# Optimization experiments

Hardware: AMD Instinct MI355X
Metric: run time of the kernel (lower is better)

The kernel has to match this reference:

```python
import jax, jax.numpy as jnp
import numpy as np

MARGIN = 0.5

def setup_inputs() -> dict:
    key = jax.random.key(0)
    k1, k2, k3, k4 = jax.random.split(key, 4)
    B, C, T, K = 16, 512, 2048, 4096
    student_out = jax.random.normal(k1, (B, C, T), dtype=jnp.float32)
    teacher_out = jax.random.normal(k2, (B, C, T), dtype=jnp.float32)
    codebook = jax.random.normal(k3, (K, C), dtype=jnp.float32)
    teacher_codes = jax.random.randint(k4, (B, T), 0, K, dtype=jnp.int64)
    return {"student_out": student_out, "teacher_out": teacher_out,
            "codebook": codebook, "teacher_codes": teacher_codes}

def _hard_negatives(student_out, codebook, teacher_codes):
    B, C, T = student_out.shape
    z = jnp.transpose(student_out, (0, 2, 1)).reshape(-1, C)  # (B*T, C)
    # squared Euclidean via expansion; sqrt-free suffices for argmin but keep faithful masking
    sq = (jnp.sum(z * z, axis=1, keepdims=True)
          + jnp.sum(codebook * codebook, axis=1)[None, :]
          - 2.0 * z @ codebook.T)                              # (B*T, K)
    dists = jnp.sqrt(jnp.maximum(sq, 0.0))
    tflat = teacher_codes.reshape(-1)
    rows = jnp.arange(tflat.shape[0])
    dists = dists.at[rows, tflat].set(jnp.inf)                 # mask correct code
    hard_idx = jnp.argmin(dists, axis=1)                       # (B*T,)
    return codebook[hard_idx].reshape(B, T, C)

def reference(student_out, teacher_out, codebook, teacher_codes):
    B, C, T = student_out.shape
    negative = _hard_negatives(student_out, codebook, teacher_codes)  # (B, T, C)
    anchor = jnp.transpose(teacher_out, (0, 2, 1))   # (B, T, C)
    positive = jnp.transpose(student_out, (0, 2, 1)) # (B, T, C)
    d_pos = jnp.linalg.norm(anchor - positive, axis=-1)  # (B, T)
    d_neg = jnp.linalg.norm(anchor - negative, axis=-1)  # (B, T)
    losses = jax.nn.relu(d_pos - d_neg + MARGIN)
    loss = losses.mean()
    d_pos_mean = d_pos.mean()
    d_neg_mean = d_neg.mean()
    margin_satisfied = (d_neg > d_pos + MARGIN).astype(jnp.float32).mean()
    return (loss, d_pos_mean, d_neg_mean, margin_satisfied)
```

## Files before the change

### kernel.cpp

```cpp
#include <hip/hip_runtime.h>
#include <math.h>

#define B_ 16
#define C_ 512
#define T_ 2048
#define K_ 4096
#define M_ (B_*T_)
#define MARGIN_ 0.5f

typedef float f32x4    __attribute__((ext_vector_type(4)));
typedef int   int32x4v __attribute__((ext_vector_type(4)));
typedef int   int32x8v __attribute__((ext_vector_type(8)));

static __device__ __forceinline__ unsigned int umin_(unsigned int a, unsigned int b) {
    return a < b ? a : b;
}
static __device__ __forceinline__ unsigned int umax_(unsigned int a, unsigned int b) {
    return a > b ? a : b;
}
static __device__ __forceinline__ void gload_lds16(const void* g, void* l) {
    __builtin_amdgcn_global_load_lds(
        (const __attribute__((address_space(1))) unsigned int*)g,
        (__attribute__((address_space(3))) unsigned int*)l,
        16, 0, 0);
}

static __device__ __forceinline__ unsigned char f32_to_e4m3(float x) {
    unsigned int u = __float_as_uint(x);
    unsigned int sgn = (u >> 24) & 0x80u;
    unsigned int ax = u & 0x7FFFFFFFu;
    if (ax >= 0x43E00000u) return (unsigned char)(sgn | 0x7Eu);
    if (ax < 0x3C800000u) {
        int q = (int)rintf(__uint_as_float(ax) * 512.0f);
        if (q >= 8) return (unsigned char)(sgn | 0x08u);
        return (unsigned char)(sgn | (unsigned)q);
    }
    unsigned int b = ax + 0x7FFFFu + ((ax >> 20) & 1u);
    unsigned int e = b >> 23;
    unsigned int m = (b >> 20) & 7u;
    int e4 = (int)e - 127 + 7;
    if (e4 >= 16) return (unsigned char)(sgn | 0x7Eu);
    return (unsigned char)(sgn | ((unsigned)e4 << 3) | m);
}

static __device__ __forceinline__ int kperm8(int o) {
    int g  = o >> 7;
    int r  = o & 127;
    int s  = (r >> 5) & 3;
    int h  = (r >> 4) & 1;
    int b8 = (r >> 3) & 1;
    return g * 128 + h * 64 + s * 16 + b8 * 8;
}

__global__ __launch_bounds__(256) void packA_kernel(
    const float* __restrict__ student, unsigned char* __restrict__ Apack)
{
    __shared__ float ts[64][65];
    const int tid = threadIdx.x;
    const int t0 = blockIdx.x * 64;
    const int c0 = blockIdx.y * 64;
    const int b  = blockIdx.z;

#pragma unroll
    for (int r = 0; r < 4; ++r) {
        int f  = tid + r * 256;
        int i  = f >> 4;
        int j4 = (f & 15) << 2;
        float4 v = *reinterpret_cast<const float4*>(
            student + ((size_t)(b * C_ + c0 + i)) * T_ + (t0 + j4));
        *reinterpret_cast<float4*>(&ts[i][j4]) = v;
    }
    __syncthreads();

#pragma unroll
    for (int r = 0; r < 2; ++r) {
        int f  = tid + r * 256;
        int j  = f >> 3;
        int pi = f & 7;
        unsigned long long w = 0ull;
#pragma unroll
        for (int u = 0; u < 8; ++u) {
            unsigned long long byte8 = (unsigned long long)f32_to_e4m3(ts[pi * 8 + u][j]);
            w |= byte8 << (8 * u);
        }
        *reinterpret_cast<unsigned long long*>(
            Apack + (size_t)(b * T_ + t0 + j) * 512 + kperm8(c0 + pi * 8)) = w;
    }
}

__global__ __launch_bounds__(256) void packB_norm_kernel(
    const float* __restrict__ cb, unsigned char* __restrict__ Bpack,
    float* __restrict__ cbnb256)
{
    int code = blockIdx.x * 4 + (threadIdx.x >> 6);
    int lane = threadIdx.x & 63;
    const float* row = cb + (size_t)code * C_;
    unsigned char* orow = Bpack + (size_t)code * 512;

    int c = lane * 8;
    float4 v0 = *reinterpret_cast<const float4*>(row + c);
    float4 v1 = *reinterpret_cast<const float4*>(row + c + 4);
    float s = v0.x*v0.x + v0.y*v0.y + v0.z*v0.z + v0.w*v0.w
            + v1.x*v1.x + v1.y*v1.y + v1.z*v1.z + v1.w*v1.w;
    unsigned long long w =
          (unsigned long long)f32_to_e4m3(v0.x)
        | ((unsigned long long)f32_to_e4m3(v0.y) << 8)
        | ((unsigned long long)f32_to_e4m3(v0.z) << 16)
        | ((unsigned long long)f32_to_e4m3(v0.w) << 24)
        | ((unsigned long long)f32_to_e4m3(v1.x) << 32)
        | ((unsigned long long)f32_to_e4m3(v1.y) << 40)
        | ((unsigned long long)f32_to_e4m3(v1.z) << 48)
        | ((unsigned long long)f32_to_e4m3(v1.w) << 56);
    *reinterpret_cast<unsigned long long*>(orow + kperm8(c)) = w;

#pragma unroll
    for (int off = 32; off; off >>= 1) s += __shfl_down(s, off);
    if (lane == 0) cbnb256[code] = (s + 1024.0f) * 256.0f;
}

__global__ __launch_bounds__(256, 2) void screen_kernel(
    const unsigned char* __restrict__ Apack,
    const unsigned char* __restrict__ Bpack,
    const float* __restrict__ cbnb256,
    uint2* __restrict__ out2)
{
    __shared__ __align__(16) unsigned char lds_tiles[4 * 2 * 128 * 64];
    __shared__ float cbnb_lds[1024];

    const int tid = threadIdx.x;
    const int l   = tid & 63;
    const int wv  = tid >> 6;
    const int wm  = wv >> 1, wn = wv & 1;
    const int lr  = l & 15;
    const int lk  = l >> 4;

    const int bid = blockIdx.x;
    const int wg  = (bid & 7) * 128 + (bid >> 3);
    const int q   = wg & 3;
    const int m0  = (wg >> 2) * 128;

    {
        float4 v = reinterpret_cast<const float4*>(cbnb256 + q * 1024)[tid];
        reinterpret_cast<float4*>(cbnb_lds)[tid] = v;
    }

    unsigned int u1[16], u2v[16];
#pragma unroll
    for (int e = 0; e < 16; ++e) { u1[e] = 0xFFFFFFFFu; u2v[e] = 0xFFFFFFFFu; }

    f32x4 acc[4][4];
#pragma unroll
    for (int i = 0; i < 4; ++i)
#pragma unroll
        for (int j = 0; j < 4; ++j) acc[i][j] = (f32x4)0.f;

    const int lane_goff = (l >> 2) * 512 + (((l & 3) ^ ((l >> 3) & 3)) * 16);
    const int r0 = wv * 32, r1 = wv * 32 + 16;

    const char* pA0 = (const char*)Apack + (size_t)m0 * 512 + lane_goff + (size_t)r0 * 512;
    const char* pA1 = (const char*)Apack + (size_t)m0 * 512 + lane_goff + (size_t)r1 * 512;
    const char* pB0 = (const char*)Bpack + (size_t)q * 524288 + lane_goff + (size_t)r0 * 512;
    const char* pB1 = (const char*)Bpack + (size_t)q * 524288 + lane_goff + (size_t)r1 * 512;

    auto stage_ptr = [&](unsigned bufbase) {
        unsigned char* Ad = &lds_tiles[bufbase];
        unsigned char* Bd = &lds_tiles[bufbase + 8192];
        gload_lds16(pA0, Ad + r0 * 64);
        gload_lds16(pA1, Ad + r1 * 64);
        gload_lds16(pB0, Bd + r0 * 64);
        gload_lds16(pB1, Bd + r1 * 64);
    };
    auto advance = [&](int s_next) {
        bool wrap = (s_next & 7) == 0;
        int dA = wrap ? -448 : 64;
        int dB = wrap ? 65088 : 64;
        pA0 += dA; pA1 += dA; pB0 += dB; pB1 += dB;
    };

    const int slotoff = (lk ^ ((lr >> 1) & 3)) * 16;

    auto compute_window = [&](unsigned bufL, unsigned bufH) {
        int32x8v a[4], bb[4];
#pragma unroll
        for (int i = 0; i < 4; ++i) {
            int ar = wm * 64 + i * 16 + lr;
            int32x4v lo = *reinterpret_cast<const int32x4v*>(
                &lds_tiles[bufL + ar * 64 + slotoff]);
            int32x4v hi = *reinterpret_cast<const int32x4v*>(
                &lds_tiles[bufH + ar * 64 + slotoff]);
            a[i] = __builtin_shufflevector(lo, hi, 0, 1, 2, 3, 4, 5, 6, 7);
        }
#pragma unroll
        for (int j = 0; j < 4; ++j) {
            int br = wn * 64 + j * 16 + lr;
            int32x4v lo = *reinterpret_cast<const int32x4v*>(
                &lds_tiles[bufL + 8192 + br * 64 + slotoff]);
            int32x4v hi = *reinterpret_cast<const int32x4v*>(
                &lds_tiles[bufH + 8192 + br * 64 + slotoff]);
            bb[j] = __builtin_shufflevector(lo, hi, 0, 1, 2, 3, 4, 5, 6, 7);
        }
#pragma unroll
        for (int i = 0; i < 4; ++i)
#pragma unroll
            for (int j = 0; j < 4; ++j)
                acc[i][j] = __builtin_amdgcn_mfma_scale_f32_16x16x128_f8f6f4(
                    a[i], bb[j], acc[i][j], 0, 0, 0, 127, 0, 127);
    };

    auto fold = [&](int ct) {
        unsigned int kk4[4];
        float cnb[4];
#pragma unroll
        for (int j = 0; j < 4; ++j) {
            int kl = ct * 128 + wn * 64 + j * 16 + lr;
            kk4[j] = (unsigned int)(q * 1024 + kl);
            cnb[j] = cbnb_lds[kl];
        }
#pragma unroll
        for (int i = 0; i < 4; ++i)
#pragma unroll
            for (int r = 0; r < 4; ++r) {
                int e = i * 4 + r;
                unsigned int p[4];
#pragma unroll
                for (int j = 0; j < 4; ++j) {
                    float s = fmaf(-512.f, acc[i][j][r], cnb[j]);
                    s = fmaxf(s, 0.f);
                    p[j] = ((unsigned int)s << 12) | kk4[j];
                }
                unsigned int mn0 = umin_(p[0], p[1]), mx0 = umax_(p[0], p[1]);
                unsigned int mn1 = umin_(p[2], p[3]), mx1 = umax_(p[2], p[3]);
                unsigned int t0 = umax_(u1[e], mn0);
                u1[e]  = umin_(u1[e], mn0);
                u2v[e] = umin_(umin_(t0, u2v[e]), mx0);
                unsigned int t1 = umax_(u1[e], mn1);
                u1[e]  = umin_(u1[e], mn1);
                u2v[e] = umin_(umin_(t1, u2v[e]), mx1);
            }
#pragma unroll
        for (int i = 0; i < 4; ++i)
#pragma unroll
            for (int j = 0; j < 4; ++j) acc[i][j] = (f32x4)0.f;
    };

    stage_ptr(0u);        advance(1);
    stage_ptr(16384u);    advance(2);

    for (int w = 0; w < 32; ++w) {
        asm volatile("s_waitcnt vmcnt(0)" ::: "memory");
        __builtin_amdgcn_s_barrier();

        if (w < 31) {
            int s2 = 2 * w + 2;
            stage_ptr((unsigned)((s2 & 3) * 16384));       advance(s2 + 1);
            stage_ptr((unsigned)(((s2 + 1) & 3) * 16384)); advance(s2 + 2);
        }

        compute_window((unsigned)(((2 * w) & 3) * 16384),
                       (unsigned)(((2 * w + 1) & 3) * 16384));
        if ((w & 3) == 3) fold(w >> 2);
    }

#pragma unroll
    for (int e = 0; e < 16; ++e) {
        unsigned int a1 = u1[e], a2 = u2v[e];
#pragma unroll
        for (int off = 1; off < 16; off <<= 1) {
            unsigned int b1 = (unsigned int)__shfl_xor((int)a1, off);
            unsigned int b2 = (unsigned int)__shfl_xor((int)a2, off);
            unsigned int m1 = umin_(a1, b1);
            a2 = umin_(umax_(a1, b1), umin_(a2, b2));
            a1 = m1;
        }
        u1[e] = a1; u2v[e] = a2;
    }

    if (lr == 0) {
        int cand = q * 2 + wn;
#pragma unroll
        for (int i = 0; i < 4; ++i)
#pragma unroll
            for (int r = 0; r < 4; ++r) {
                int m = m0 + wm * 64 + i * 16 + lk * 4 + r;
                out2[(size_t)cand * M_ + m] = make_uint2(u1[i * 4 + r], u2v[i * 4 + r]);
            }
    }
}

__global__ __launch_bounds__(256) void loss_kernel(
    const float* __restrict__ student, const float* __restrict__ teacher,
    const float* __restrict__ cb, const uint2* __restrict__ out2,
    const int* __restrict__ codes, float* __restrict__ partials)
{
    __shared__ float sh[4][64][5];

    const int l  = threadIdx.x & 63;
    const int qw = threadIdx.x >> 6;
    const int m  = blockIdx.x * 64 + l;
    const int b  = m / T_;
    const int t  = m % T_;

    uint2 g = out2[m];
#pragma unroll
    for (int c = 1; c < 8; ++c) {
        uint2 o = out2[(size_t)c * M_ + m];
        unsigned int m1 = umin_(g.x, o.x);
        g.y = umin_(umax_(g.x, o.x), umin_(g.y, o.y));
        g.x = m1;
    }
    const int k1 = (int)(g.x & 0xFFFu);
    const int k2 = (int)(g.y & 0xFFFu);

    const float* sp = student + (size_t)b * C_ * T_ + t;
    const float* tp = teacher + (size_t)b * C_ * T_ + t;
    const float4* c1p = reinterpret_cast<const float4*>(cb + (size_t)k1 * C_);
    const float4* c2p = reinterpret_cast<const float4*>(cb + (size_t)k2 * C_);

    float dp = 0.f, ds1 = 0.f, ds2 = 0.f, dt1 = 0.f, dt2 = 0.f;
    const int c4beg = qw * 32;
#pragma unroll 4
    for (int c4 = c4beg; c4 < c4beg + 32; ++c4) {
        float4 cv1 = c1p[c4];
        float4 cv2 = c2p[c4];
        float a0 = tp[(size_t)(c4 * 4 + 0) * T_];
        float a1 = tp[(size_t)(c4 * 4 + 1) * T_];
        float a2 = tp[(size_t)(c4 * 4 + 2) * T_];
        float a3 = tp[(size_t)(c4 * 4 + 3) * T_];
        float p0 = sp[(size_t)(c4 * 4 + 0) * T_];
        float p1 = sp[(size_t)(c4 * 4 + 1) * T_];
        float p2 = sp[(size_t)(c4 * 4 + 2) * T_];
        float p3 = sp[(size_t)(c4 * 4 + 3) * T_];
        float e;
        e = a0 - p0;   dp  = fmaf(e, e, dp);
        e = a1 - p1;   dp  = fmaf(e, e, dp);
        e = a2 - p2;   dp  = fmaf(e, e, dp);
        e = a3 - p3;   dp  = fmaf(e, e, dp);
        e = p0 - cv1.x; ds1 = fmaf(e, e, ds1);
        e = p1 - cv1.y; ds1 = fmaf(e, e, ds1);
        e = p2 - cv1.z; ds1 = fmaf(e, e, ds1);
        e = p3 - cv1.w; ds1 = fmaf(e, e, ds1);
        e = p0 - cv2.x; ds2 = fmaf(e, e, ds2);
        e = p1 - cv2.y; ds2 = fmaf(e, e, ds2);
        e = p2 - cv2.z; ds2 = fmaf(e, e, ds2);
        e = p3 - cv2.w; ds2 = fmaf(e, e, ds2);
        e = a0 - cv1.x; dt1 = fmaf(e, e, dt1);
        e = a1 - cv1.y; dt1 = fmaf(e, e, dt1);
        e = a2 - cv1.z; dt1 = fmaf(e, e, dt1);
        e = a3 - cv1.w; dt1 = fmaf(e, e, dt1);
        e = a0 - cv2.x; dt2 = fmaf(e, e, dt2);
        e = a1 - cv2.y; dt2 = fmaf(e, e, dt2);
        e = a2 - cv2.z; dt2 = fmaf(e, e, dt2);
        e = a3 - cv2.w; dt2 = fmaf(e, e, dt2);
    }
    sh[qw][l][0] = dp;
    sh[qw][l][1] = ds1;
    sh[qw][l][2] = ds2;
    sh[qw][l][3] = dt1;
    sh[qw][l][4] = dt2;
    __syncthreads();

    if (qw == 0) {
        float S0 = 0.f, S1 = 0.f, S2 = 0.f, S3 = 0.f, S4 = 0.f;
#pragma unroll
        for (int w = 0; w < 4; ++w) {
            S0 += sh[w][l][0];
            S1 += sh[w][l][1];
            S2 += sh[w][l][2];
            S3 += sh[w][l][3];
            S4 += sh[w][l][4];
        }
        const int tc = codes[m];
        bool v1 = (k1 != tc), v2 = (k2 != tc);
        bool take2;
        if (!v1)      take2 = true;
        else if (!v2) take2 = false;
        else          take2 = (S2 < S1) || (S2 == S1 && k2 < k1);
        float dn = take2 ? S4 : S3;

        float dpos = sqrtf(S0);
        float dneg = sqrtf(dn);
        float loss = fmaxf(dpos - dneg + MARGIN_, 0.f);
        float ind  = (dneg > dpos + MARGIN_) ? 1.f : 0.f;

        float v0 = loss, vv1 = dpos, vv2 = dneg, vv3 = ind;
#pragma unroll
        for (int off = 32; off; off >>= 1) {
            v0  += __shfl_down(v0, off);
            vv1 += __shfl_down(vv1, off);
            vv2 += __shfl_down(vv2, off);
            vv3 += __shfl_down(vv3, off);
        }
        if (l == 0) {
            partials[blockIdx.x * 4 + 0] = v0;
            partials[blockIdx.x * 4 + 1] = vv1;
            partials[blockIdx.x * 4 + 2] = vv2;
            partials[blockIdx.x * 4 + 3] = vv3;
        }
    }
}

__global__ __launch_bounds__(256) void final_kernel(
    const float* __restrict__ partials, float* __restrict__ out)
{
    __shared__ float sh[4][4];
    int tid = threadIdx.x;
    float s0 = partials[tid * 4 + 0] + partials[(tid + 256) * 4 + 0];
    float s1 = partials[tid * 4 + 1] + partials[(tid + 256) * 4 + 1];
    float s2 = partials[tid * 4 + 2] + partials[(tid + 256) * 4 + 2];
    float s3 = partials[tid * 4 + 3] + partials[(tid + 256) * 4 + 3];
#pragma unroll
    for (int off = 32; off; off >>= 1) {
        s0 += __shfl_down(s0, off);
        s1 += __shfl_down(s1, off);
        s2 += __shfl_down(s2, off);
        s3 += __shfl_down(s3, off);
    }
    int w = tid >> 6, lane = tid & 63;
    if (lane == 0) { sh[w][0] = s0; sh[w][1] = s1; sh[w][2] = s2; sh[w][3] = s3; }
    __syncthreads();
    if (tid == 0) {
        const float inv = 1.0f / (float)M_;
        float o0 = 0.f, o1 = 0.f, o2 = 0.f, o3 = 0.f;
#pragma unroll
        for (int ww = 0; ww < 4; ++ww) {
            o0 += sh[ww][0]; o1 += sh[ww][1]; o2 += sh[ww][2]; o3 += sh[ww][3];
        }
        out[0] = o0 * inv;
        out[1] = o1 * inv;
        out[2] = o2 * inv;
        out[3] = o3 * inv;
    }
}

extern "C" void kernel_launch(void* const* d_in, const int* in_sizes, int n_in,
                              void* d_out, int out_size, void* d_ws, size_t ws_size,
                              hipStream_t stream)
{
    (void)in_sizes; (void)n_in; (void)out_size; (void)ws_size;
    const float* student = (const float*)d_in[0];
    const float* teacher = (const float*)d_in[1];
    const float* cb      = (const float*)d_in[2];
    const int*   codes   = (const int*)d_in[3];
    float* out = (float*)d_out;
    char* ws = (char*)d_ws;

    const size_t OFF_APACK = 0;
    const size_t OFF_BPACK = (size_t)M_ * 512;
    const size_t OFF_CBN   = OFF_BPACK + (size_t)K_ * 512;
    const size_t OFF_OUT2  = OFF_CBN + K_ * 4;
    const size_t OFF_PARTS = OFF_OUT2 + (size_t)8 * M_ * 8;

    unsigned char* Apack = (unsigned char*)(ws + OFF_APACK);
    unsigned char* Bpack = (unsigned char*)(ws + OFF_BPACK);
    float* cbnb  = (float*)(ws + OFF_CBN);
    uint2* out2  = (uint2*)(ws + OFF_OUT2);
    float* parts = (float*)(ws + OFF_PARTS);

    packA_kernel<<<dim3(T_ / 64, C_ / 64, B_), 256, 0, stream>>>(student, Apack);
    packB_norm_kernel<<<K_ / 4, 256, 0, stream>>>(cb, Bpack, cbnb);
    screen_kernel<<<1024, 256, 0, stream>>>(Apack, Bpack, cbnb, out2);
    loss_kernel<<<M_ / 64, 256, 0, stream>>>(student, teacher, cb, out2, codes, parts);
    final_kernel<<<1, 256, 0, stream>>>(parts, out);
}
```

Before: 153.9 us.

## Load A fragments directly from global into registers, stage only B in LDS

Stops staging the A (activation) tile through LDS. Each wave now loads its own A fragments straight from global memory into registers and double-buffers them across loop iterations, while only the codebook B tile goes through the LDS ring. This halves LDS footprint and removes the A LDS writes and reads. In exchange, the two column waves sharing the same A rows now each fetch them from global/L2, and the extra register buffers raise register pressure under the two-blocks-per-CU launch bound.

```diff
diff --git a/kernel.cpp b/kernel.cpp
--- a/kernel.cpp
+++ b/kernel.cpp
@@ -124,7 +124,7 @@
     const float* __restrict__ cbnb256,
     uint2* __restrict__ out2)
 {
-    __shared__ __align__(16) unsigned char lds_tiles[4 * 2 * 128 * 64];
+    __shared__ __align__(16) unsigned char lds_tiles[4 * 128 * 64];
     __shared__ float cbnb_lds[1024];
 
     const int tid = threadIdx.x;
@@ -157,46 +157,44 @@
     const int lane_goff = (l >> 2) * 512 + (((l & 3) ^ ((l >> 3) & 3)) * 16);
     const int r0 = wv * 32, r1 = wv * 32 + 16;
 
-    const char* pA0 = (const char*)Apack + (size_t)m0 * 512 + lane_goff + (size_t)r0 * 512;
-    const char* pA1 = (const char*)Apack + (size_t)m0 * 512 + lane_goff + (size_t)r1 * 512;
     const char* pB0 = (const char*)Bpack + (size_t)q * 524288 + lane_goff + (size_t)r0 * 512;
     const char* pB1 = (const char*)Bpack + (size_t)q * 524288 + lane_goff + (size_t)r1 * 512;
 
     auto stage_ptr = [&](unsigned bufbase) {
-        unsigned char* Ad = &lds_tiles[bufbase];
-        unsigned char* Bd = &lds_tiles[bufbase + 8192];
-        gload_lds16(pA0, Ad + r0 * 64);
-        gload_lds16(pA1, Ad + r1 * 64);
+        unsigned char* Bd = &lds_tiles[bufbase];
         gload_lds16(pB0, Bd + r0 * 64);
         gload_lds16(pB1, Bd + r1 * 64);
     };
     auto advance = [&](int s_next) {
         bool wrap = (s_next & 7) == 0;
-        int dA = wrap ? -448 : 64;
         int dB = wrap ? 65088 : 64;
-        pA0 += dA; pA1 += dA; pB0 += dB; pB1 += dB;
+        pB0 += dB; pB1 += dB;
     };
 
+    const unsigned char* pAlane =
+        Apack + (size_t)(m0 + wm * 64 + lr) * 512 + lk * 16;
+
+    auto loadA = [&](int g, int32x8v* a) {
+#pragma unroll
+        for (int i = 0; i < 4; ++i) {
+            const unsigned char* p = pAlane + (size_t)i * 8192 + g * 128;
+            int32x4v lo = *reinterpret_cast<const int32x4v*>(p);
+            int32x4v hi = *reinterpret_cast<const int32x4v*>(p + 64);
+            a[i] = __builtin_shufflevector(lo, hi, 0, 1, 2, 3, 4, 5, 6, 7);
+        }
+    };
+
     const int slotoff = (lk ^ ((lr >> 1) & 3)) * 16;
 
-    auto compute_window = [&](unsigned bufL, unsigned bufH) {
-        int32x8v a[4], bb[4];
-#pragma unroll
-        for (int i = 0; i < 4; ++i) {
-            int ar = wm * 64 + i * 16 + lr;
-            int32x4v lo = *reinterpret_cast<const int32x4v*>(
-                &lds_tiles[bufL + ar * 64 + slotoff]);
-            int32x4v hi = *reinterpret_cast<const int32x4v*>(
-                &lds_tiles[bufH + ar * 64 + slotoff]);
-            a[i] = __builtin_shufflevector(lo, hi, 0, 1, 2, 3, 4, 5, 6, 7);
-        }
+    auto compute_window = [&](unsigned bufL, unsigned bufH, const int32x8v* a) {
+        int32x8v bb[4];
 #pragma unroll
         for (int j = 0; j < 4; ++j) {
             int br = wn * 64 + j * 16 + lr;
             int32x4v lo = *reinterpret_cast<const int32x4v*>(
-                &lds_tiles[bufL + 8192 + br * 64 + slotoff]);
+                &lds_tiles[bufL + br * 64 + slotoff]);
             int32x4v hi = *reinterpret_cast<const int32x4v*>(
-                &lds_tiles[bufH + 8192 + br * 64 + slotoff]);
+                &lds_tiles[bufH + br * 64 + slotoff]);
             bb[j] = __builtin_shufflevector(lo, hi, 0, 1, 2, 3, 4, 5, 6, 7);
         }
 #pragma unroll
@@ -243,22 +241,31 @@
             for (int j = 0; j < 4; ++j) acc[i][j] = (f32x4)0.f;
     };
 
-    stage_ptr(0u);        advance(1);
-    stage_ptr(16384u);    advance(2);
-
+    stage_ptr(0u);       advance(1);
+    stage_ptr(8192u);    advance(2);
+    int32x8v a_cur[4], a_next[4];
+    loadA(0, a_cur);
+
+#pragma unroll 4
     for (int w = 0; w < 32; ++w) {
         asm volatile("s_waitcnt vmcnt(0)" ::: "memory");
         __builtin_amdgcn_s_barrier();
 
         if (w < 31) {
             int s2 = 2 * w + 2;
-            stage_ptr((unsigned)((s2 & 3) * 16384));       advance(s2 + 1);
-            stage_ptr((unsigned)(((s2 + 1) & 3) * 16384)); advance(s2 + 2);
-        }
-
-        compute_window((unsigned)(((2 * w) & 3) * 16384),
-                       (unsigned)(((2 * w + 1) & 3) * 16384));
+            stage_ptr((unsigned)((s2 & 3) * 8192));       advance(s2 + 1);
+            stage_ptr((unsigned)(((s2 + 1) & 3) * 8192)); advance(s2 + 2);
+            loadA((w + 1) & 3, a_next);
+        }
+
+        compute_window((unsigned)(((2 * w) & 3) * 8192),
+                       (unsigned)(((2 * w + 1) & 3) * 8192), a_cur);
         if ((w & 3) == 3) fold(w >> 2);
+
+        if (w < 31) {
+#pragma unroll
+            for (int i = 0; i < 4; ++i) a_cur[i] = a_next[i];
+        }
     }
 
 #pragma unroll
```

Result: slower. 492.3 us (+219.9%).
